# Optimization experiments

Measured on AMD Instinct MI355X. Metric: run time of the kernel, lower is better.

The kernel has to match this reference:

```python
import jax, jax.numpy as jnp
import numpy as np
import math

H = 1e-4  # finite-difference step
TW = math.pi / 8.0  # transition width
LOW = math.pi / 2.0 - TW
HIGH = math.pi / 2.0 + TW


def _smooth_step(t):
    # equivalent to torch smooth_step with masks: 0 below LOW, 1 above HIGH,
    x = jnp.clip((t - LOW) / (HIGH - LOW), 0.0, 1.0)
    return x * x * (3.0 - 2.0 * x)


def _compute_potential(xyz, a_param, b_param, direction):
    # xyz: [B,3]
    a = jnp.clip(a_param, 0.0, 20.0)
    b = jnp.clip(b_param, 0.0, 20.0)
    r2 = jnp.sum(xyz * xyz, axis=1)          # [B]
    r = jnp.sqrt(r2)
    origin = r == 0.0
    safe_r = jnp.where(origin, 1.0, r)
    p_hat = xyz / safe_r[:, None]            # [B,3]
    dot = p_hat @ direction                  # [B]
    theta = jnp.arccos(jnp.clip(dot, -1.0, 1.0))
    w = _smooth_step(theta)
    # w*direct + (1-w)*ray = 0.5*a*r^2 + (1-w)*0.5*b*r^2*theta^2
    pot = 0.5 * a * r2 + (1.0 - w) * 0.5 * b * r2 * theta * theta
    return jnp.where(origin, 0.0, pot)


def setup_inputs() -> dict:
    key = jax.random.key(0)
    B = 8388608
    xyz = jax.random.normal(key, (B, 3), dtype=jnp.float32)
    theta_dir, phi_dir = 1.0471975511965976, 0.7853981633974483
    direction = jnp.array([
        math.sin(theta_dir) * math.cos(phi_dir),
        math.sin(theta_dir) * math.sin(phi_dir),
        math.cos(theta_dir),
    ], dtype=jnp.float32)
    a_param = jnp.float32(1.0)
    b_param = jnp.float32(10.0)
    return {"xyz": xyz, "a_param": a_param, "b_param": b_param, "direction": direction}


def reference(xyz, a_param, b_param, direction):
    # compute_velocity: central finite differences of the potential, negated
    eye = jnp.eye(3, dtype=xyz.dtype)
    grads = []
    for i in range(3):  # fixed tiny loop over xyz axes
        u_plus = _compute_potential(xyz + H * eye[i], a_param, b_param, direction)
        u_minus = _compute_potential(xyz - H * eye[i], a_param, b_param, direction)
        grads.append((u_plus - u_minus) / (2.0 * H))
    velocity = -jnp.stack(grads, axis=1)  # [B,3]
    return velocity
```

## Files before the change

kernel.cpp:

```cpp
#include <hip/hip_runtime.h>
#include <math.h>

#define LOW_F   1.1780972450961724f
#define INV_TW  1.2732395447351628f
#define WP_K    7.639437268410977f

typedef float floatx4 __attribute__((ext_vector_type(4)));

__device__ __forceinline__ float fast_acos(float x) {
    float s = __builtin_fabsf(x);
    bool big = s > 0.5f;
    float z = big ? fmaf(-0.5f, s, 0.5f) : x * x;
    float r = big ? __builtin_amdgcn_sqrtf(z) : s;
    float p = fmaf(z, 4.2163199048e-2f, 2.4181311049e-2f);
    p = fmaf(z, p, 4.5470025998e-2f);
    p = fmaf(z, p, 7.4953002686e-2f);
    p = fmaf(z, p, 1.6666752422e-1f);
    float asn = fmaf(r * z, p, r);
    float t2 = 2.0f * asn;
    float rb = (x >= 0.0f) ? t2 : (3.14159274f - t2);
    float rs = (x >= 0.0f) ? (1.57079637f - asn) : (1.57079637f + asn);
    return big ? rb : rs;
}

__device__ __forceinline__ void point_velocity(float x, float y, float z,
                                               float a, float b,
                                               float dx, float dy, float dz,
                                               float& vx, float& vy, float& vz) {
    float r2 = x * x + y * y + z * z;
    float r = __builtin_amdgcn_sqrtf(r2);
    float invr = __builtin_amdgcn_rcpf(r);
    float dot = (x * dx + y * dy + z * dz) * invr;
    dot = fminf(fmaxf(dot, -1.0f), 1.0f);
    float theta = fast_acos(dot);

    float t = (theta - LOW_F) * INV_TW;
    t = fminf(fmaxf(t, 0.0f), 1.0f);
    float w = t * t * (3.0f - 2.0f * t);
    float one_m_w = 1.0f - w;
    float wp = WP_K * t * (1.0f - t);

    float th2 = theta * theta;
    float k1 = fmaf(b * th2, one_m_w, a);

    float sin2 = fmaf(-dot, dot, 1.0f);
    float sinth = __builtin_amdgcn_sqrtf(fmaxf(sin2, 0.0f));
    float rcpsin = __builtin_amdgcn_rcpf(fmaxf(sinth, 1e-30f));
    float num = fmaf(2.0f * theta, one_m_w, -th2 * wp);
    float k2 = (r * 0.5f * b) * num * rcpsin;

    float m = dot * invr;
    float gx = fmaf(-m, x, dx);
    float gy = fmaf(-m, y, dy);
    float gz = fmaf(-m, z, dz);

    float ovx = fmaf(-k1, x, k2 * gx);
    float ovy = fmaf(-k1, y, k2 * gy);
    float ovz = fmaf(-k1, z, k2 * gz);

    bool origin = (r2 == 0.0f);
    vx = origin ? 0.0f : ovx;
    vy = origin ? 0.0f : ovy;
    vz = origin ? 0.0f : ovz;
}

extern "C" __global__ void __launch_bounds__(256, 2)
canyon3d_pipe_kernel(const float* __restrict__ xyz,
                     const float* __restrict__ a_param,
                     const float* __restrict__ b_param,
                     const float* __restrict__ dir,
                     float* __restrict__ out,
                     int B) {
    int nquad = B >> 2;
    int tid = blockIdx.x * blockDim.x + threadIdx.x;
    int stride = gridDim.x * blockDim.x;

    float a = fminf(fmaxf(a_param[0], 0.0f), 20.0f);
    float b = fminf(fmaxf(b_param[0], 0.0f), 20.0f);
    float dx = dir[0], dy = dir[1], dz = dir[2];

    const floatx4* in4 = (const floatx4*)xyz;
    floatx4* out4 = (floatx4*)out;

    if (tid < nquad) {
        int q = tid;
        floatx4 A  = in4[3 * q + 0];
        floatx4 Bv = in4[3 * q + 1];
        floatx4 C  = in4[3 * q + 2];
        int qn = q + stride;
        for (;;) {
            int qp = (qn < nquad) ? qn : q;
            floatx4 An = in4[3 * qp + 0];
            floatx4 Bn = in4[3 * qp + 1];
            floatx4 Cn = in4[3 * qp + 2];

            float o0, o1, o2, o3, o4, o5, o6, o7, o8, o9, o10, o11;
            point_velocity(A.x, A.y, A.z,   a, b, dx, dy, dz, o0, o1, o2);
            point_velocity(A.w, Bv.x, Bv.y, a, b, dx, dy, dz, o3, o4, o5);
            point_velocity(Bv.z, Bv.w, C.x, a, b, dx, dy, dz, o6, o7, o8);
            point_velocity(C.y, C.z, C.w,   a, b, dx, dy, dz, o9, o10, o11);

            floatx4 O0 = {o0, o1, o2, o3};
            floatx4 O1 = {o4, o5, o6, o7};
            floatx4 O2 = {o8, o9, o10, o11};
            out4[3 * q + 0] = O0;
            out4[3 * q + 1] = O1;
            out4[3 * q + 2] = O2;

            if (qn >= nquad) break;
            q = qn; qn += stride;
            A = An; Bv = Bn; C = Cn;
        }
    }

    int done = nquad << 2;
    int rem = B - done;
    if (tid < rem) {
        int i = done + tid;
        float x = xyz[3 * i], y = xyz[3 * i + 1], z = xyz[3 * i + 2];
        float vx, vy, vz;
        point_velocity(x, y, z, a, b, dx, dy, dz, vx, vy, vz);
        out[3 * i] = vx; out[3 * i + 1] = vy; out[3 * i + 2] = vz;
    }
}

extern "C" void kernel_launch(void* const* d_in, const int* in_sizes, int n_in,
                              void* d_out, int out_size, void* d_ws, size_t ws_size,
                              hipStream_t stream) {
    const float* xyz = (const float*)d_in[0];
    const float* a_param = (const float*)d_in[1];
    const float* b_param = (const float*)d_in[2];
    const float* dir = (const float*)d_in[3];
    float* out = (float*)d_out;

    int B = in_sizes[0] / 3;
    int nquad = (B + 3) / 4;
    int blocks = 1024;
    int maxBlocks = (nquad + 255) / 256;
    if (blocks > maxBlocks) blocks = maxBlocks > 0 ? maxBlocks : 1;
    canyon3d_pipe_kernel<<<dim3(blocks), dim3(256), 0, stream>>>(xyz, a_param, b_param, dir, out, B);
}
```

Baseline: 188.6 us.

## Batch four quads per iteration with all loads issued up front

Replaces the one-ahead software-prefetch loop with a grid-stride loop that loads four strided quads (12 float4 loads) before any compute, using a sched_barrier to keep all loads ahead of the math. The aim is more memory-level parallelism per thread so DRAM latency is hidden on this bandwidth-bound kernel. It also drops the minBlocks=2 launch bound and doubles the grid to 2048 blocks, which shifts register pressure and occupancy.

Measured after the change: 186.0 us. About the same (-1.4%).

```diff
diff --git a/kernel.cpp b/kernel.cpp
--- a/kernel.cpp
+++ b/kernel.cpp
@@ -64,16 +64,34 @@
     vz = origin ? 0.0f : ovz;
 }
 
-extern "C" __global__ void __launch_bounds__(256, 2)
-canyon3d_pipe_kernel(const float* __restrict__ xyz,
-                     const float* __restrict__ a_param,
-                     const float* __restrict__ b_param,
-                     const float* __restrict__ dir,
-                     float* __restrict__ out,
-                     int B) {
+__device__ __forceinline__ void do_quad(floatx4 A, floatx4 Bv, floatx4 C,
+                                        float a, float b,
+                                        float dx, float dy, float dz,
+                                        floatx4* __restrict__ out4, int q) {
+    float o0, o1, o2, o3, o4, o5, o6, o7, o8, o9, o10, o11;
+    point_velocity(A.x, A.y, A.z,   a, b, dx, dy, dz, o0, o1, o2);
+    point_velocity(A.w, Bv.x, Bv.y, a, b, dx, dy, dz, o3, o4, o5);
+    point_velocity(Bv.z, Bv.w, C.x, a, b, dx, dy, dz, o6, o7, o8);
+    point_velocity(C.y, C.z, C.w,   a, b, dx, dy, dz, o9, o10, o11);
+    floatx4 O0 = {o0, o1, o2, o3};
+    floatx4 O1 = {o4, o5, o6, o7};
+    floatx4 O2 = {o8, o9, o10, o11};
+    out4[3 * q + 0] = O0;
+    out4[3 * q + 1] = O1;
+    out4[3 * q + 2] = O2;
+}
+
+extern "C" __global__ void __launch_bounds__(256)
+canyon3d_batch4_kernel(const float* __restrict__ xyz,
+                       const float* __restrict__ a_param,
+                       const float* __restrict__ b_param,
+                       const float* __restrict__ dir,
+                       float* __restrict__ out,
+                       int B) {
     int nquad = B >> 2;
     int tid = blockIdx.x * blockDim.x + threadIdx.x;
     int stride = gridDim.x * blockDim.x;
+    int bigstride = stride << 2;
 
     float a = fminf(fmaxf(a_param[0], 0.0f), 20.0f);
     float b = fminf(fmaxf(b_param[0], 0.0f), 20.0f);
@@ -82,35 +100,26 @@
     const floatx4* in4 = (const floatx4*)xyz;
     floatx4* out4 = (floatx4*)out;
 
-    if (tid < nquad) {
-        int q = tid;
-        floatx4 A  = in4[3 * q + 0];
-        floatx4 Bv = in4[3 * q + 1];
-        floatx4 C  = in4[3 * q + 2];
-        int qn = q + stride;
-        for (;;) {
-            int qp = (qn < nquad) ? qn : q;
-            floatx4 An = in4[3 * qp + 0];
-            floatx4 Bn = in4[3 * qp + 1];
-            floatx4 Cn = in4[3 * qp + 2];
+    for (int qb = tid; qb < nquad; qb += bigstride) {
+        int q0 = qb;
+        int q1 = qb + stride;
+        int q2 = qb + 2 * stride;
+        int q3 = qb + 3 * stride;
+        bool v1 = q1 < nquad, v2 = q2 < nquad, v3 = q3 < nquad;
+        int c1 = v1 ? q1 : q0;
+        int c2 = v2 ? q2 : q0;
+        int c3 = v3 ? q3 : q0;
 
-            float o0, o1, o2, o3, o4, o5, o6, o7, o8, o9, o10, o11;
-            point_velocity(A.x, A.y, A.z,   a, b, dx, dy, dz, o0, o1, o2);
-            point_velocity(A.w, Bv.x, Bv.y, a, b, dx, dy, dz, o3, o4, o5);
-            point_velocity(Bv.z, Bv.w, C.x, a, b, dx, dy, dz, o6, o7, o8);
-            point_velocity(C.y, C.z, C.w,   a, b, dx, dy, dz, o9, o10, o11);
+        floatx4 A0 = in4[3 * q0 + 0], B0 = in4[3 * q0 + 1], C0 = in4[3 * q0 + 2];
+        floatx4 A1 = in4[3 * c1 + 0], B1 = in4[3 * c1 + 1], C1 = in4[3 * c1 + 2];
+        floatx4 A2 = in4[3 * c2 + 0], B2 = in4[3 * c2 + 1], C2 = in4[3 * c2 + 2];
+        floatx4 A3 = in4[3 * c3 + 0], B3 = in4[3 * c3 + 1], C3 = in4[3 * c3 + 2];
+        __builtin_amdgcn_sched_barrier(0);
 
-            floatx4 O0 = {o0, o1, o2, o3};
-            floatx4 O1 = {o4, o5, o6, o7};
-            floatx4 O2 = {o8, o9, o10, o11};
-            out4[3 * q + 0] = O0;
-            out4[3 * q + 1] = O1;
-            out4[3 * q + 2] = O2;
-
-            if (qn >= nquad) break;
-            q = qn; qn += stride;
-            A = An; Bv = Bn; C = Cn;
-        }
+        do_quad(A0, B0, C0, a, b, dx, dy, dz, out4, q0);
+        if (v1) do_quad(A1, B1, C1, a, b, dx, dy, dz, out4, q1);
+        if (v2) do_quad(A2, B2, C2, a, b, dx, dy, dz, out4, q2);
+        if (v3) do_quad(A3, B3, C3, a, b, dx, dy, dz, out4, q3);
     }
 
     int done = nquad << 2;
@@ -135,8 +144,8 @@
 
     int B = in_sizes[0] / 3;
     int nquad = (B + 3) / 4;
-    int blocks = 1024;
+    int blocks = 2048;
     int maxBlocks = (nquad + 255) / 256;
     if (blocks > maxBlocks) blocks = maxBlocks > 0 ? maxBlocks : 1;
-    canyon3d_pipe_kernel<<<dim3(blocks), dim3(256), 0, stream>>>(xyz, a_param, b_param, dir, out, B);
+    canyon3d_batch4_kernel<<<dim3(blocks), dim3(256), 0, stream>>>(xyz, a_param, b_param, dir, out, B);
 }
```
